# Performance work log

Measured on AMD Instinct MI355X. Metric: run time of the kernel, lower is better.

## Reference

```python
import jax, jax.numpy as jnp
import numpy as np

B, T = 1, 2048
N_EMBD = 2048
N_HEAD = 16
HEAD_DIM = 128
Q_COMP = 1536
KV_COMP = 512
ROT = 64  # rotate_dim


def setup_inputs() -> dict:
    key = jax.random.key(0)
    ks = jax.random.split(key, 12)
    nrm = lambda k, shp, sc=1.0: jax.random.normal(k, shp, jnp.float32) * sc
    return {
        "x": nrm(ks[0], (B, T, N_EMBD)),
        "cos": jax.random.uniform(ks[1], (T, ROT // 2), jnp.float32),
        "sin": jax.random.uniform(ks[2], (T, ROT // 2), jnp.float32),
        "Wq_d_w": nrm(ks[3], (Q_COMP, N_EMBD), 0.02),
        "Wq_d_b": jnp.zeros((Q_COMP,), jnp.float32),
        "Wkv_d_w": nrm(ks[4], (KV_COMP, N_EMBD), 0.02),
        "Wq_u_w": nrm(ks[5], (N_HEAD * HEAD_DIM, Q_COMP), 0.02),
        "Wk_u_w": nrm(ks[6], (N_HEAD * HEAD_DIM, KV_COMP), 0.02),
        "Wv_u_w": nrm(ks[7], (N_HEAD * HEAD_DIM, KV_COMP), 0.02),
        "W_qr_w": nrm(ks[8], (N_HEAD * ROT, Q_COMP), 0.02),
        "W_kr_w": nrm(ks[9], (ROT, N_EMBD), 0.02),
        "W_out_w": nrm(ks[10], (N_EMBD, N_HEAD * HEAD_DIM), 0.02),
    }


def _rope(x, cos, sin):
    # x: [B, H, T, r]; cos/sin: [T, r//2] broadcast over batch and heads
    d = x.shape[-1] // 2
    x1, x2 = x[..., :d], x[..., d:]
    return jnp.concatenate([x1 * cos + x2 * sin, -x1 * sin + x2 * cos], axis=-1)


def reference(x, cos, sin, Wq_d_w, Wq_d_b, Wkv_d_w, Wq_u_w, Wk_u_w, Wv_u_w, W_qr_w, W_kr_w, W_out_w):
    Bn, Tn, _ = x.shape
    cq = x @ Wq_d_w.T + Wq_d_b           # [B,T,Qc] latent query
    ckv = x @ Wkv_d_w.T                  # [B,T,Kc] compressed KV latent (= K_t = V)
    Wq_u = Wq_u_w.reshape(N_HEAD, HEAD_DIM, Q_COMP)
    Wk_u = Wk_u_w.reshape(N_HEAD, HEAD_DIM, KV_COMP)
    Wv_u = Wv_u_w.reshape(N_HEAD, HEAD_DIM, KV_COMP)
    # absorbed per-head W_qk[h] = Wq_u_h^T @ Wk_u_h : [H, Qc, Kc]
    W_qk = jnp.einsum('hdq,hdk->hqk', Wq_u, Wk_u)
    Q_t = jnp.einsum('btq,hqk->bhtk', cq, W_qk)   # [B,H,T,Kc] content query in latent space
    Q_r = _rope(jnp.einsum('btq,hrq->bhtr', cq, W_qr_w.reshape(N_HEAD, ROT, Q_COMP)), cos, sin)
    K_r = _rope((x @ W_kr_w.T)[:, None], cos, sin)  # [B,1,T,R] single shared rotary key head
    Q = jnp.concatenate([Q_t, Q_r], axis=-1)        # [B,H,T,Kc+R]
    K = jnp.concatenate([ckv[:, None], K_r], axis=-1)  # [B,1,T,Kc+R]
    scale = 1.0 / np.sqrt(KV_COMP + ROT).astype(np.float32)
    scores = jnp.einsum('bhqd,bokd->bhqk', Q, K) * scale  # [B,H,T,T]
    causal = jnp.tril(jnp.ones((Tn, Tn), dtype=bool))
    scores = jnp.where(causal, scores, jnp.asarray(-1e30, scores.dtype))
    probs = jax.nn.softmax(scores, axis=-1)
    attn = jnp.einsum('bhqk,bkc->bhqc', probs, ckv)  # [B,H,T,Kc] latent attention output
    # absorbed output projection: up-project per head via Wv_u, then W_out
    heads = jnp.einsum('bhtc,hdc->bthd', attn, Wv_u).reshape(Bn, Tn, N_HEAD * HEAD_DIM)
    return heads @ W_out_w.T                          # [B,T,C]
```

## Files before the change

kernel.cpp:

```cpp
#include <hip/hip_runtime.h>
#include <math.h>
#include <stdint.h>
#include <stddef.h>

typedef __bf16 bf16;
typedef __bf16 bf16x8 __attribute__((ext_vector_type(8)));
typedef __bf16 bf16x4 __attribute__((ext_vector_type(4)));
typedef __bf16 bf16x2 __attribute__((ext_vector_type(2)));
typedef float  f32x4  __attribute__((ext_vector_type(4)));
typedef float  f32x4v __attribute__((ext_vector_type(4)));

typedef __attribute__((address_space(1))) const void* as1cv;
typedef __attribute__((address_space(3))) void*       as3v;

__device__ __forceinline__ f32x4 mfma16(bf16x8 a, bf16x8 b, f32x4 c) {
  return __builtin_amdgcn_mfma_f32_16x16x32_bf16(a, b, c, 0, 0, 0);
}

__device__ __forceinline__ void gload_lds16(const bf16* g, bf16* l) {
  __builtin_amdgcn_global_load_lds((as1cv)g, (as3v)l, 16, 0, 0);
}

struct CvtTable {
  const float* s[9];
  bf16* d[9];
  int cum[10];
};

__global__ void cvt_all(CvtTable T, int total4) {
  int i = blockIdx.x * blockDim.x + threadIdx.x;
  int stride = gridDim.x * blockDim.x;
  for (; i < total4; i += stride) {
    int k = 0;
#pragma unroll
    for (int j = 1; j < 9; ++j) k += (i >= T.cum[j]) ? 1 : 0;
    int off = i - T.cum[k];
    f32x4v v = ((const f32x4v*)T.s[k])[off];
    bf16x4 o;
    o[0] = (bf16)v[0]; o[1] = (bf16)v[1]; o[2] = (bf16)v[2]; o[3] = (bf16)v[3];
    ((bf16x4*)T.d[k])[off] = o;
  }
}

__device__ __forceinline__ void gemm_core(
    const bf16* __restrict__ A, int lda,
    const bf16* __restrict__ B, int K,
    float* __restrict__ Cf, bf16* __restrict__ Cb, int ldc,
    const float* __restrict__ bias, int bias_n, int m0, int n0)
{
  __shared__ __align__(16) bf16 Al[2][128 * 64];
  __shared__ __align__(16) bf16 Bl[2][128 * 64];
  const int tid = threadIdx.x;
  const int l = tid & 63;
  const int wid = tid >> 6;
  const int wr = wid >> 2, wc = wid & 3;
  const int lr = l & 15, lg = l >> 4;

  const int ch0 = tid, ch1 = tid + 512;
  const int ar0 = ch0 >> 3, ap0 = (ch0 & 7) ^ (ar0 & 7);
  const int ar1 = ch1 >> 3, ap1 = (ch1 & 7) ^ (ar1 & 7);
  const bf16* pA0 = A + (size_t)(m0 + ar0) * lda + ap0 * 8;
  const bf16* pA1 = A + (size_t)(m0 + ar1) * lda + ap1 * 8;
  const bf16* pB0 = B + (size_t)(n0 + ar0) * K + ap0 * 8;
  const bf16* pB1 = B + (size_t)(n0 + ar1) * K + ap1 * 8;
  bf16* dA0[2] = { &Al[0][ch0 * 8], &Al[1][ch0 * 8] };
  bf16* dA1[2] = { &Al[0][ch1 * 8], &Al[1][ch1 * 8] };
  bf16* dB0[2] = { &Bl[0][ch0 * 8], &Bl[1][ch0 * 8] };
  bf16* dB1[2] = { &Bl[0][ch1 * 8], &Bl[1][ch1 * 8] };

  auto STAGE = [&](int b) {
    gload_lds16(pA0, b ? dA0[1] : dA0[0]);
    gload_lds16(pA1, b ? dA1[1] : dA1[0]);
    gload_lds16(pB0, b ? dB0[1] : dB0[0]);
    gload_lds16(pB1, b ? dB1[1] : dB1[0]);
    pA0 += 64; pA1 += 64; pB0 += 64; pB1 += 64;
  };

  f32x4 z = {0.f, 0.f, 0.f, 0.f};
  f32x4 acc[4][2];
#pragma unroll
  for (int i = 0; i < 4; ++i)
#pragma unroll
    for (int j = 0; j < 2; ++j) acc[i][j] = z;

  STAGE(0);
  int cur = 0;
  for (int k0 = 0; k0 < K; k0 += 64) {
    if (k0 + 64 < K) {
      STAGE(cur ^ 1);
      asm volatile("s_waitcnt vmcnt(4)" ::: "memory");
    } else {
      asm volatile("s_waitcnt vmcnt(0)" ::: "memory");
    }
    __builtin_amdgcn_s_barrier();
    __builtin_amdgcn_sched_barrier(0);
#pragma unroll
    for (int kk = 0; kk < 2; ++kk) {
      bf16x8 af[4], bfr[2];
#pragma unroll
      for (int i = 0; i < 4; ++i) {
        int row = wr * 64 + i * 16 + lr;
        int cq = kk * 4 + lg;
        af[i] = *(const bf16x8*)(&Al[cur][row * 64 + ((cq ^ (row & 7)) * 8)]);
      }
#pragma unroll
      for (int j = 0; j < 2; ++j) {
        int row = wc * 32 + j * 16 + lr;
        int cq = kk * 4 + lg;
        bfr[j] = *(const bf16x8*)(&Bl[cur][row * 64 + ((cq ^ (row & 7)) * 8)]);
      }
#pragma unroll
      for (int i = 0; i < 4; ++i)
#pragma unroll
        for (int j = 0; j < 2; ++j)
          acc[i][j] = mfma16(af[i], bfr[j], acc[i][j]);
    }
    __builtin_amdgcn_sched_barrier(0);
    __builtin_amdgcn_s_barrier();
    cur ^= 1;
  }

#pragma unroll
  for (int i = 0; i < 4; ++i)
#pragma unroll
    for (int j = 0; j < 2; ++j)
#pragma unroll
      for (int r = 0; r < 4; ++r) {
        int row = m0 + wr * 64 + i * 16 + lg * 4 + r;
        int col = n0 + wc * 32 + j * 16 + lr;
        float v = acc[i][j][r];
        if (bias != nullptr && col < bias_n) v += bias[col];
        if (Cf != nullptr) Cf[(size_t)row * ldc + col] = v;
        else               Cb[(size_t)row * ldc + col] = (bf16)v;
      }
}

template<bool OUTF32>
__global__ __launch_bounds__(512) void gemm_bt(
    const bf16* __restrict__ A, int lda,
    const bf16* __restrict__ B, int K,
    float* __restrict__ Cf, bf16* __restrict__ Cb, int ldc,
    const float* __restrict__ bias, int bias_n)
{
  gemm_core(A, lda, B, K, OUTF32 ? Cf : nullptr, Cb, ldc, bias, bias_n,
            blockIdx.y * 128, blockIdx.x * 128);
}

__global__ __launch_bounds__(512) void gemm_bt_dual(
    const bf16* __restrict__ A0, int lda0, const bf16* __restrict__ B0, int K0,
    bf16* __restrict__ C0, int ldc0, int nbx0,
    const bf16* __restrict__ A1, int lda1, const bf16* __restrict__ B1, int K1,
    bf16* __restrict__ C1, int ldc1, int nbx1)
{
  int bid = blockIdx.x;
  if (bid < nbx0 * 16) {
    gemm_core(A0, lda0, B0, K0, nullptr, C0, ldc0, nullptr, 0,
              (bid / nbx0) * 128, (bid % nbx0) * 128);
  } else {
    bid -= nbx0 * 16;
    gemm_core(A1, lda1, B1, K1, nullptr, C1, ldc1, nullptr, 0,
              (bid / nbx1) * 128, (bid % nbx1) * 128);
  }
}

__global__ void rope_tv(const bf16* __restrict__ QA, const bf16* __restrict__ c_all,
                        const float* __restrict__ cosb, const float* __restrict__ sinb,
                        bf16* __restrict__ Qr, bf16* __restrict__ Kr,
                        const bf16* __restrict__ KV, bf16* __restrict__ Vt)
{
  int bid = blockIdx.x;
  if (bid < 2048) {
    int t = bid;
    for (int idx = threadIdx.x; idx < 544; idx += 256) {
      if (idx < 512) {
        int h = idx >> 5, p = idx & 31;
        float x1 = (float)QA[(size_t)t * 3072 + 2048 + h * 64 + p];
        float x2 = (float)QA[(size_t)t * 3072 + 2048 + h * 64 + 32 + p];
        float c = cosb[t * 32 + p], s = sinb[t * 32 + p];
        Qr[(size_t)t * 1024 + h * 64 + p]      = (bf16)( x1 * c + x2 * s);
        Qr[(size_t)t * 1024 + h * 64 + 32 + p] = (bf16)(-x1 * s + x2 * c);
      } else {
        int p = idx - 512;
        float x1 = (float)c_all[(size_t)t * 2176 + 2048 + p];
        float x2 = (float)c_all[(size_t)t * 2176 + 2048 + 32 + p];
        float c = cosb[t * 32 + p], s = sinb[t * 32 + p];
        Kr[(size_t)t * 64 + p]      = (bf16)( x1 * c + x2 * s);
        Kr[(size_t)t * 64 + 32 + p] = (bf16)(-x1 * s + x2 * c);
      }
    }
  } else {
    __shared__ bf16 tile[32][33];
    int tb = bid - 2048;
    int t0 = (tb & 63) * 32, c0 = (tb >> 6) * 32;
    int tx = threadIdx.x & 31, ty = threadIdx.x >> 5;
#pragma unroll
    for (int r = 0; r < 4; ++r)
      tile[ty + r * 8][tx] = KV[(size_t)(t0 + ty + r * 8) * 4096 + 2048 + c0 + tx];
    __syncthreads();
#pragma unroll
    for (int r = 0; r < 4; ++r)
      Vt[(size_t)(c0 + ty + r * 8) * 2048 + t0 + tx] = tile[tx][ty + r * 8];
  }
}

__global__ __launch_bounds__(256) void attn_kernel(
    const bf16* __restrict__ QA,
    const bf16* __restrict__ Qr,
    const bf16* __restrict__ KV,
    const bf16* __restrict__ Kr,
    const bf16* __restrict__ Vt,
    bf16* __restrict__ heads)
{
  __shared__ __align__(16) bf16 Kl[2][32 * 128];
  __shared__ __align__(16) bf16 Krl[2][32 * 64];
  __shared__ __align__(16) bf16 Vl[2][128 * 32];
  __shared__ __align__(16) bf16 Pl[4][16][40];

  const int tid = threadIdx.x;
  const int l = tid & 63;
  const int wid = tid >> 6;
  const int lr = l & 15, lg = l >> 4;

  const int wg = blockIdx.x;
  const int xcd = wg & 7, inx = wg >> 3;
  const int half = inx >> 5, j = inx & 31;
  const int h = xcd * 2 + half;
  const int qb = half ? j : 31 - j;
  const int q0 = qb * 64 + wid * 16;
  const int q = q0 + lr;

  const float scale = 0.041666666666666664f;
  f32x4 z = {0.f, 0.f, 0.f, 0.f};

  const int chK0 = tid, chK1 = tid + 256;
  const int rK0 = chK0 >> 4, pK0 = chK0 & 15;
  const int rK1 = chK1 >> 4, pK1 = chK1 & 15;
  const int cbK0 = (pK0 & 8) | ((pK0 & 7) ^ (rK0 & 7));
  const int cbK1 = (pK1 & 8) | ((pK1 & 7) ^ (rK1 & 7));
  const bf16* gK0 = &KV[(size_t)rK0 * 4096 + h * 128 + cbK0 * 8];
  const bf16* gK1 = &KV[(size_t)rK1 * 4096 + h * 128 + cbK1 * 8];
  const int rKr = tid >> 3, pKr = tid & 7, cbKr = pKr ^ (rKr & 7);
  const bf16* gKr = &Kr[(size_t)rKr * 64 + cbKr * 8];
  const int chV0 = tid, chV1 = tid + 256;
  const int rV0 = chV0 >> 2, pV0 = chV0 & 3, cbV0 = pV0 ^ ((rV0 >> 1) & 3);
  const int rV1 = chV1 >> 2, pV1 = chV1 & 3, cbV1 = pV1 ^ ((rV1 >> 1) & 3);
  const bf16* gV0 = &Vt[(size_t)(h * 128 + rV0) * 2048 + cbV0 * 8];
  const bf16* gV1 = &Vt[(size_t)(h * 128 + rV1) * 2048 + cbV1 * 8];
  bf16* dK0[2] = { &Kl[0][chK0 * 8], &Kl[1][chK0 * 8] };
  bf16* dK1[2] = { &Kl[0][chK1 * 8], &Kl[1][chK1 * 8] };
  bf16* dKr[2] = { &Krl[0][tid * 8], &Krl[1][tid * 8] };
  bf16* dV0[2] = { &Vl[0][chV0 * 8], &Vl[1][chV0 * 8] };
  bf16* dV1[2] = { &Vl[0][chV1 * 8], &Vl[1][chV1 * 8] };

  auto STAGE = [&](int b) {
    gload_lds16(gK0, b ? dK0[1] : dK0[0]);
    gload_lds16(gK1, b ? dK1[1] : dK1[0]);
    gload_lds16(gKr, b ? dKr[1] : dKr[0]);
    gload_lds16(gV0, b ? dV0[1] : dV0[0]);
    gload_lds16(gV1, b ? dV1[1] : dV1[0]);
    gK0 += 32 * 4096; gK1 += 32 * 4096; gKr += 32 * 64; gV0 += 32; gV1 += 32;
  };

  bf16x8 aq[6];
#pragma unroll
  for (int kc = 0; kc < 4; ++kc)
    aq[kc] = *(const bf16x8*)&QA[(size_t)q * 3072 + h * 128 + kc * 32 + lg * 8];
#pragma unroll
  for (int kc = 4; kc < 6; ++kc)
    aq[kc] = *(const bf16x8*)&Qr[(size_t)q * 1024 + h * 64 + (kc - 4) * 32 + lg * 8];

  float m_run = -1e30f, l_run = 0.f;
  f32x4 acc[8];
#pragma unroll
  for (int c = 0; c < 8; ++c) acc[c] = z;

  const int nIter = 2 * qb + 2;
  STAGE(0);
  int cur = 0;
  for (int st = 0; st < nIter; ++st) {
    const int s0 = st * 32;
    if (st + 1 < nIter) {
      STAGE(cur ^ 1);
      asm volatile("s_waitcnt vmcnt(5)" ::: "memory");
    } else {
      asm volatile("s_waitcnt vmcnt(0)" ::: "memory");
    }
    __builtin_amdgcn_s_barrier();
    __builtin_amdgcn_sched_barrier(0);
    if (s0 <= q0 + 15) {
      f32x4 sc[2];
      sc[0] = z; sc[1] = z;
#pragma unroll
      for (int t = 0; t < 2; ++t) {
        const int rr = t * 16 + lr;
#pragma unroll
        for (int kc = 0; kc < 4; ++kc) {
          int g = kc * 4 + lg;
          bf16x8 ka = *(const bf16x8*)&Kl[cur][rr * 128 + (((g & 8) | ((g & 7) ^ (rr & 7))) * 8)];
          sc[t] = mfma16(ka, aq[kc], sc[t]);
        }
#pragma unroll
        for (int kc = 4; kc < 6; ++kc) {
          int g = (kc - 4) * 4 + lg;
          bf16x8 ka = *(const bf16x8*)&Krl[cur][rr * 64 + ((g ^ (rr & 7)) * 8)];
          sc[t] = mfma16(ka, aq[kc], sc[t]);
        }
      }
      float pv[2][4];
      float mx = -1e30f;
      if (s0 + 31 > q0) {
#pragma unroll
        for (int t = 0; t < 2; ++t)
#pragma unroll
          for (int r = 0; r < 4; ++r) {
            int k = s0 + t * 16 + lg * 4 + r;
            float v = sc[t][r] * scale;
            if (k > q) v = -1e30f;
            pv[t][r] = v;
            mx = fmaxf(mx, v);
          }
      } else {
#pragma unroll
        for (int t = 0; t < 2; ++t)
#pragma unroll
          for (int r = 0; r < 4; ++r) {
            float v = sc[t][r] * scale;
            pv[t][r] = v;
            mx = fmaxf(mx, v);
          }
      }
      mx = fmaxf(mx, __shfl_xor(mx, 16, 64));
      mx = fmaxf(mx, __shfl_xor(mx, 32, 64));
      if (!__all(mx - m_run <= 8.f)) {
        float mnew = fmaxf(m_run, mx);
        float alpha = __expf(m_run - mnew);
        l_run *= alpha;
#pragma unroll
        for (int c = 0; c < 8; ++c)
#pragma unroll
          for (int r = 0; r < 4; ++r) acc[c][r] *= alpha;
        m_run = mnew;
      }
      float sum = 0.f;
#pragma unroll
      for (int t = 0; t < 2; ++t)
#pragma unroll
        for (int r = 0; r < 4; ++r) {
          float e = __expf(pv[t][r] - m_run);
          pv[t][r] = e;
          sum += e;
        }
      sum += __shfl_xor(sum, 16, 64);
      sum += __shfl_xor(sum, 32, 64);
      l_run += sum;
#pragma unroll
      for (int t = 0; t < 2; ++t)
#pragma unroll
        for (int hf = 0; hf < 2; ++hf) {
          bf16x2 w;
          w[0] = (bf16)pv[t][2 * hf];
          w[1] = (bf16)pv[t][2 * hf + 1];
          *(bf16x2*)&Pl[wid][lr][t * 16 + lg * 4 + 2 * hf] = w;
        }
      bf16x8 pa = *(const bf16x8*)&Pl[wid][lr][lg * 8];
#pragma unroll
      for (int c = 0; c < 8; ++c) {
        int rv = c * 16 + lr;
        bf16x8 va = *(const bf16x8*)&Vl[cur][rv * 32 + ((lg ^ ((rv >> 1) & 3)) * 8)];
        acc[c] = mfma16(va, pa, acc[c]);
      }
    }
    __builtin_amdgcn_sched_barrier(0);
    __builtin_amdgcn_s_barrier();
    cur ^= 1;
  }

  const float inv = 1.f / l_run;
#pragma unroll
  for (int c = 0; c < 8; ++c) {
    bf16x4 o;
#pragma unroll
    for (int r = 0; r < 4; ++r) o[r] = (bf16)(acc[c][r] * inv);
    *(bf16x4*)&heads[(size_t)q * 2048 + h * 128 + c * 16 + lg * 4] = o;
  }
}

extern "C" void kernel_launch(void* const* d_in, const int* in_sizes, int n_in,
                              void* d_out, int out_size, void* d_ws, size_t ws_size,
                              hipStream_t stream) {
  (void)in_sizes; (void)n_in; (void)out_size; (void)ws_size;
  const float* x      = (const float*)d_in[0];
  const float* cosp   = (const float*)d_in[1];
  const float* sinp   = (const float*)d_in[2];
  const float* Wq_d   = (const float*)d_in[3];
  const float* Wq_d_b = (const float*)d_in[4];
  const float* Wkv_d  = (const float*)d_in[5];
  const float* Wq_u   = (const float*)d_in[6];
  const float* Wk_u   = (const float*)d_in[7];
  const float* Wv_u   = (const float*)d_in[8];
  const float* W_qr   = (const float*)d_in[9];
  const float* W_kr   = (const float*)d_in[10];
  const float* W_out  = (const float*)d_in[11];

  char* ws = (char*)d_ws;
  size_t off = 0;
  auto alloc = [&](size_t bytes) {
    char* p = ws + off;
    off += (bytes + 255) & ~(size_t)255;
    return p;
  };
  bf16* xb    = (bf16*)alloc((size_t)2048 * 2048 * 2);
  bf16* Wcat  = (bf16*)alloc((size_t)2176 * 2048 * 2);
  bf16* c_all = (bf16*)alloc((size_t)2048 * 2176 * 2);
  bf16* Wqu   = (bf16*)alloc((size_t)3072 * 1536 * 2);
  bf16* QA    = (bf16*)alloc((size_t)2048 * 3072 * 2);
  bf16* Wkvu  = (bf16*)alloc((size_t)4096 * 512 * 2);
  bf16* KV    = (bf16*)alloc((size_t)2048 * 4096 * 2);
  bf16* Qr    = (bf16*)alloc((size_t)2048 * 1024 * 2);
  bf16* Kr    = (bf16*)alloc((size_t)2048 * 64 * 2);
  bf16* Wout  = (bf16*)alloc((size_t)2048 * 2048 * 2);
  bf16* Vt    = xb;
  bf16* heads = Wqu;

  CvtTable T;
  const float* srcs[9] = { x, Wq_d, Wkv_d, W_kr, Wq_u, W_qr, Wk_u, Wv_u, W_out };
  bf16* dsts[9] = { xb, Wcat, Wcat + (size_t)1536 * 2048, Wcat + (size_t)2048 * 2048,
                    Wqu, Wqu + (size_t)2048 * 1536, Wkvu, Wkvu + (size_t)2048 * 512, Wout };
  size_t ns[9] = { (size_t)2048 * 2048, (size_t)1536 * 2048, (size_t)512 * 2048,
                   (size_t)64 * 2048, (size_t)2048 * 1536, (size_t)1024 * 1536,
                   (size_t)2048 * 512, (size_t)2048 * 512, (size_t)2048 * 2048 };
  int cum = 0;
  for (int i = 0; i < 9; ++i) {
    T.s[i] = srcs[i]; T.d[i] = dsts[i]; T.cum[i] = cum;
    cum += (int)(ns[i] / 4);
  }
  T.cum[9] = cum;
  cvt_all<<<2048, 256, 0, stream>>>(T, cum);

  gemm_bt<false><<<dim3(17, 16), 512, 0, stream>>>(xb, 2048, Wcat, 2048,
                                                   nullptr, c_all, 2176, Wq_d_b, 1536);
  gemm_bt_dual<<<24 * 16 + 32 * 16, 512, 0, stream>>>(
      c_all, 2176, Wqu, 1536, QA, 3072, 24,
      c_all + 1536, 2176, Wkvu, 512, KV, 4096, 32);
  rope_tv<<<2048 + 4096, 256, 0, stream>>>(QA, c_all, cosp, sinp, Qr, Kr, KV, Vt);
  attn_kernel<<<512, 256, 0, stream>>>(QA, Qr, KV, Kr, Vt, heads);
  gemm_bt<true><<<dim3(16, 16), 512, 0, stream>>>(heads, 2048, Wout, 2048,
                                                  (float*)d_out, nullptr, 2048, nullptr, 0);
}
```

Measured before the change: 318.5 us.

## Split-K the down and output GEMMs and retile attention into 32-row blocks

The two large GEMMs are split along K into two grid halves that write partial results, followed by separate reduction kernels (adding the bias for the query latent). The GEMM inner loop replaces the manual vmcnt waits with plain __syncthreads, which may reduce load/compute overlap. The attention kernel now uses 128-thread blocks covering 32 query rows with a balanced causal ordering, a unified LDS buffer for K, rotary K and V, and register shuffles in place of the LDS round-trip for P. The partial-sum scheme doubles grid occupancy but adds extra kernels and partial-sum memory traffic, and the first GEMM's partials are rounded to bf16 before summation.

```diff
diff --git a/kernel.cpp b/kernel.cpp
--- a/kernel.cpp
+++ b/kernel.cpp
@@ -44,7 +44,7 @@
 
 __device__ __forceinline__ void gemm_core(
     const bf16* __restrict__ A, int lda,
-    const bf16* __restrict__ B, int K,
+    const bf16* __restrict__ B, int ldb, int Klen,
     float* __restrict__ Cf, bf16* __restrict__ Cb, int ldc,
     const float* __restrict__ bias, int bias_n, int m0, int n0)
 {
@@ -61,8 +61,8 @@
   const int ar1 = ch1 >> 3, ap1 = (ch1 & 7) ^ (ar1 & 7);
   const bf16* pA0 = A + (size_t)(m0 + ar0) * lda + ap0 * 8;
   const bf16* pA1 = A + (size_t)(m0 + ar1) * lda + ap1 * 8;
-  const bf16* pB0 = B + (size_t)(n0 + ar0) * K + ap0 * 8;
-  const bf16* pB1 = B + (size_t)(n0 + ar1) * K + ap1 * 8;
+  const bf16* pB0 = B + (size_t)(n0 + ar0) * ldb + ap0 * 8;
+  const bf16* pB1 = B + (size_t)(n0 + ar1) * ldb + ap1 * 8;
   bf16* dA0[2] = { &Al[0][ch0 * 8], &Al[1][ch0 * 8] };
   bf16* dA1[2] = { &Al[0][ch1 * 8], &Al[1][ch1 * 8] };
   bf16* dB0[2] = { &Bl[0][ch0 * 8], &Bl[1][ch0 * 8] };
@@ -84,16 +84,10 @@
     for (int j = 0; j < 2; ++j) acc[i][j] = z;
 
   STAGE(0);
+  __syncthreads();
   int cur = 0;
-  for (int k0 = 0; k0 < K; k0 += 64) {
-    if (k0 + 64 < K) {
-      STAGE(cur ^ 1);
-      asm volatile("s_waitcnt vmcnt(4)" ::: "memory");
-    } else {
-      asm volatile("s_waitcnt vmcnt(0)" ::: "memory");
-    }
-    __builtin_amdgcn_s_barrier();
-    __builtin_amdgcn_sched_barrier(0);
+  for (int k0 = 0; k0 < Klen; k0 += 64) {
+    if (k0 + 64 < Klen) STAGE(cur ^ 1);
 #pragma unroll
     for (int kk = 0; kk < 2; ++kk) {
       bf16x8 af[4], bfr[2];
@@ -115,8 +109,7 @@
         for (int j = 0; j < 2; ++j)
           acc[i][j] = mfma16(af[i], bfr[j], acc[i][j]);
     }
-    __builtin_amdgcn_sched_barrier(0);
-    __builtin_amdgcn_s_barrier();
+    __syncthreads();
     cur ^= 1;
   }
 
@@ -136,14 +129,17 @@
 }
 
 template<bool OUTF32>
-__global__ __launch_bounds__(512) void gemm_bt(
+__global__ __launch_bounds__(512) void gemm_splitk(
     const bf16* __restrict__ A, int lda,
-    const bf16* __restrict__ B, int K,
-    float* __restrict__ Cf, bf16* __restrict__ Cb, int ldc,
-    const float* __restrict__ bias, int bias_n)
-{
-  gemm_core(A, lda, B, K, OUTF32 ? Cf : nullptr, Cb, ldc, bias, bias_n,
-            blockIdx.y * 128, blockIdx.x * 128);
+    const bf16* __restrict__ B, int ldb, int Khalf,
+    float* __restrict__ F0, float* __restrict__ F1,
+    bf16* __restrict__ H0, bf16* __restrict__ H1, int ldc)
+{
+  int zz = blockIdx.z;
+  gemm_core(A + zz * Khalf, lda, B + zz * Khalf, ldb, Khalf,
+            OUTF32 ? (zz ? F1 : F0) : nullptr,
+            OUTF32 ? nullptr : (zz ? H1 : H0), ldc,
+            nullptr, 0, blockIdx.y * 128, blockIdx.x * 128);
 }
 
 __global__ __launch_bounds__(512) void gemm_bt_dual(
@@ -154,12 +150,50 @@
 {
   int bid = blockIdx.x;
   if (bid < nbx0 * 16) {
-    gemm_core(A0, lda0, B0, K0, nullptr, C0, ldc0, nullptr, 0,
+    gemm_core(A0, lda0, B0, K0, K0, nullptr, C0, ldc0, nullptr, 0,
               (bid / nbx0) * 128, (bid % nbx0) * 128);
   } else {
     bid -= nbx0 * 16;
-    gemm_core(A1, lda1, B1, K1, nullptr, C1, ldc1, nullptr, 0,
+    gemm_core(A1, lda1, B1, K1, K1, nullptr, C1, ldc1, nullptr, 0,
               (bid / nbx1) * 128, (bid % nbx1) * 128);
+  }
+}
+
+__global__ void reduce_c(const bf16* __restrict__ P0, const bf16* __restrict__ P1,
+                         const float* __restrict__ bias, bf16* __restrict__ c_all)
+{
+  const int n8 = 2048 * 2176 / 8;
+  int i = blockIdx.x * blockDim.x + threadIdx.x;
+  int stride = gridDim.x * blockDim.x;
+  for (; i < n8; i += stride) {
+    int col8 = (i % 272) * 8;
+    bf16x8 a = ((const bf16x8*)P0)[i];
+    bf16x8 b = ((const bf16x8*)P1)[i];
+    bf16x8 o;
+    if (col8 < 1536) {
+#pragma unroll
+      for (int j = 0; j < 8; ++j)
+        o[j] = (bf16)((float)a[j] + (float)b[j] + bias[col8 + j]);
+    } else {
+#pragma unroll
+      for (int j = 0; j < 8; ++j)
+        o[j] = (bf16)((float)a[j] + (float)b[j]);
+    }
+    ((bf16x8*)c_all)[i] = o;
+  }
+}
+
+__global__ void reduce_f(const float* __restrict__ P0, const float* __restrict__ P1,
+                         float* __restrict__ out)
+{
+  const int n4 = 2048 * 2048 / 4;
+  int i = blockIdx.x * blockDim.x + threadIdx.x;
+  int stride = gridDim.x * blockDim.x;
+  for (; i < n4; i += stride) {
+    f32x4v a = ((const f32x4v*)P0)[i];
+    f32x4v b = ((const f32x4v*)P1)[i];
+    f32x4v o = a + b;
+    ((f32x4v*)out)[i] = o;
   }
 }
 
@@ -203,7 +237,7 @@
   }
 }
 
-__global__ __launch_bounds__(256) void attn_kernel(
+__global__ __launch_bounds__(128) void attn_kernel(
     const bf16* __restrict__ QA,
     const bf16* __restrict__ Qr,
     const bf16* __restrict__ KV,
@@ -211,10 +245,7 @@
     const bf16* __restrict__ Vt,
     bf16* __restrict__ heads)
 {
-  __shared__ __align__(16) bf16 Kl[2][32 * 128];
-  __shared__ __align__(16) bf16 Krl[2][32 * 64];
-  __shared__ __align__(16) bf16 Vl[2][128 * 32];
-  __shared__ __align__(16) bf16 Pl[4][16][40];
+  __shared__ __align__(16) bf16 L[2][10240];
 
   const int tid = threadIdx.x;
   const int l = tid & 63;
@@ -223,42 +254,46 @@
 
   const int wg = blockIdx.x;
   const int xcd = wg & 7, inx = wg >> 3;
-  const int half = inx >> 5, j = inx & 31;
-  const int h = xcd * 2 + half;
-  const int qb = half ? j : 31 - j;
-  const int q0 = qb * 64 + wid * 16;
+  const int rnd = inx >> 5, c = inx & 31;
+  const int h = xcd * 2 + (rnd >> 1);
+  const int qt = (rnd == 0) ? (63 - c) : (rnd == 1) ? (31 - c) : (rnd == 2) ? c : (32 + c);
+  const int q0 = qt * 32 + wid * 16;
   const int q = q0 + lr;
 
   const float scale = 0.041666666666666664f;
   f32x4 z = {0.f, 0.f, 0.f, 0.f};
 
-  const int chK0 = tid, chK1 = tid + 256;
-  const int rK0 = chK0 >> 4, pK0 = chK0 & 15;
-  const int rK1 = chK1 >> 4, pK1 = chK1 & 15;
-  const int cbK0 = (pK0 & 8) | ((pK0 & 7) ^ (rK0 & 7));
-  const int cbK1 = (pK1 & 8) | ((pK1 & 7) ^ (rK1 & 7));
-  const bf16* gK0 = &KV[(size_t)rK0 * 4096 + h * 128 + cbK0 * 8];
-  const bf16* gK1 = &KV[(size_t)rK1 * 4096 + h * 128 + cbK1 * 8];
-  const int rKr = tid >> 3, pKr = tid & 7, cbKr = pKr ^ (rKr & 7);
-  const bf16* gKr = &Kr[(size_t)rKr * 64 + cbKr * 8];
-  const int chV0 = tid, chV1 = tid + 256;
-  const int rV0 = chV0 >> 2, pV0 = chV0 & 3, cbV0 = pV0 ^ ((rV0 >> 1) & 3);
-  const int rV1 = chV1 >> 2, pV1 = chV1 & 3, cbV1 = pV1 ^ ((rV1 >> 1) & 3);
-  const bf16* gV0 = &Vt[(size_t)(h * 128 + rV0) * 2048 + cbV0 * 8];
-  const bf16* gV1 = &Vt[(size_t)(h * 128 + rV1) * 2048 + cbV1 * 8];
-  bf16* dK0[2] = { &Kl[0][chK0 * 8], &Kl[1][chK0 * 8] };
-  bf16* dK1[2] = { &Kl[0][chK1 * 8], &Kl[1][chK1 * 8] };
-  bf16* dKr[2] = { &Krl[0][tid * 8], &Krl[1][tid * 8] };
-  bf16* dV0[2] = { &Vl[0][chV0 * 8], &Vl[1][chV0 * 8] };
-  bf16* dV1[2] = { &Vl[0][chV1 * 8], &Vl[1][chV1 * 8] };
+  const bf16* gK[6]; int sK[6]; int chK[6];
+#pragma unroll
+  for (int i = 0; i < 6; ++i) {
+    int ch = i * 128 + tid;
+    int row = ch / 24, gcol = ch - row * 24;
+    int lgc = (gcol & 24) | ((gcol & 7) ^ (row & 7));
+    if (lgc < 16) { gK[i] = KV + (size_t)row * 4096 + h * 128 + lgc * 8; sK[i] = 32 * 4096; }
+    else          { gK[i] = Kr + (size_t)row * 64 + (lgc - 16) * 8;      sK[i] = 32 * 64; }
+    chK[i] = ch;
+  }
+  const bf16* gV[4]; int chV[4];
+#pragma unroll
+  for (int j = 0; j < 4; ++j) {
+    int ch = j * 128 + tid;
+    int r = ch >> 2, p = ch & 3;
+    int cb = p ^ ((r >> 1) & 3);
+    gV[j] = Vt + (size_t)(h * 128 + r) * 2048 + cb * 8;
+    chV[j] = ch;
+  }
 
   auto STAGE = [&](int b) {
-    gload_lds16(gK0, b ? dK0[1] : dK0[0]);
-    gload_lds16(gK1, b ? dK1[1] : dK1[0]);
-    gload_lds16(gKr, b ? dKr[1] : dKr[0]);
-    gload_lds16(gV0, b ? dV0[1] : dV0[0]);
-    gload_lds16(gV1, b ? dV1[1] : dV1[0]);
-    gK0 += 32 * 4096; gK1 += 32 * 4096; gKr += 32 * 64; gV0 += 32; gV1 += 32;
+#pragma unroll
+    for (int i = 0; i < 6; ++i) {
+      gload_lds16(gK[i], &L[b][chK[i] * 8]);
+      gK[i] += sK[i];
+    }
+#pragma unroll
+    for (int j = 0; j < 4; ++j) {
+      gload_lds16(gV[j], &L[b][6144 + chV[j] * 8]);
+      gV[j] += 32;
+    }
   };
 
   bf16x8 aq[6];
@@ -269,107 +304,126 @@
   for (int kc = 4; kc < 6; ++kc)
     aq[kc] = *(const bf16x8*)&Qr[(size_t)q * 1024 + h * 64 + (kc - 4) * 32 + lg * 8];
 
+  const int sl0 = lr + 16 * ((lg & 1) * 2);
+  const int sl1 = sl0 + 16;
+  const bool hiT = (lg >> 1) != 0;
+
   float m_run = -1e30f, l_run = 0.f;
   f32x4 acc[8];
 #pragma unroll
-  for (int c = 0; c < 8; ++c) acc[c] = z;
-
-  const int nIter = 2 * qb + 2;
+  for (int cc = 0; cc < 8; ++cc) acc[cc] = z;
+
+  const int nIter = qt + 1;
   STAGE(0);
   int cur = 0;
   for (int st = 0; st < nIter; ++st) {
     const int s0 = st * 32;
     if (st + 1 < nIter) {
       STAGE(cur ^ 1);
-      asm volatile("s_waitcnt vmcnt(5)" ::: "memory");
+      asm volatile("s_waitcnt vmcnt(10)" ::: "memory");
     } else {
       asm volatile("s_waitcnt vmcnt(0)" ::: "memory");
     }
     __builtin_amdgcn_s_barrier();
     __builtin_amdgcn_sched_barrier(0);
-    if (s0 <= q0 + 15) {
-      f32x4 sc[2];
-      sc[0] = z; sc[1] = z;
-#pragma unroll
-      for (int t = 0; t < 2; ++t) {
-        const int rr = t * 16 + lr;
-#pragma unroll
-        for (int kc = 0; kc < 4; ++kc) {
-          int g = kc * 4 + lg;
-          bf16x8 ka = *(const bf16x8*)&Kl[cur][rr * 128 + (((g & 8) | ((g & 7) ^ (rr & 7))) * 8)];
-          sc[t] = mfma16(ka, aq[kc], sc[t]);
+
+    f32x4 scA[2], scB[2];
+    scA[0] = z; scA[1] = z; scB[0] = z; scB[1] = z;
+#pragma unroll
+    for (int t = 0; t < 2; ++t) {
+      const int rr = t * 16 + lr;
+#pragma unroll
+      for (int kc = 0; kc < 6; ++kc) {
+        int g = kc * 4 + lg;
+        int gc = (g & 24) | ((g & 7) ^ (rr & 7));
+        bf16x8 ka = *(const bf16x8*)&L[cur][rr * 192 + gc * 8];
+        if (kc < 3) scA[t] = mfma16(ka, aq[kc], scA[t]);
+        else        scB[t] = mfma16(ka, aq[kc], scB[t]);
+      }
+    }
+    bf16x8 va[8];
+#pragma unroll
+    for (int cc = 0; cc < 8; ++cc) {
+      int rv = cc * 16 + lr;
+      va[cc] = *(const bf16x8*)&L[cur][6144 + rv * 32 + ((lg ^ ((rv >> 1) & 3)) * 8)];
+    }
+    f32x4 sc[2];
+    sc[0] = scA[0] + scB[0];
+    sc[1] = scA[1] + scB[1];
+
+    float pv[2][4];
+    float mx = -1e30f;
+    if (s0 + 31 > q0) {
+#pragma unroll
+      for (int t = 0; t < 2; ++t)
+#pragma unroll
+        for (int r = 0; r < 4; ++r) {
+          int k = s0 + t * 16 + lg * 4 + r;
+          float v = sc[t][r] * scale;
+          if (k > q) v = -1e30f;
+          pv[t][r] = v;
+          mx = fmaxf(mx, v);
         }
-#pragma unroll
-        for (int kc = 4; kc < 6; ++kc) {
-          int g = (kc - 4) * 4 + lg;
-          bf16x8 ka = *(const bf16x8*)&Krl[cur][rr * 64 + ((g ^ (rr & 7)) * 8)];
-          sc[t] = mfma16(ka, aq[kc], sc[t]);
+    } else {
+#pragma unroll
+      for (int t = 0; t < 2; ++t)
+#pragma unroll
+        for (int r = 0; r < 4; ++r) {
+          float v = sc[t][r] * scale;
+          pv[t][r] = v;
+          mx = fmaxf(mx, v);
         }
-      }
-      float pv[2][4];
-      float mx = -1e30f;
-      if (s0 + 31 > q0) {
-#pragma unroll
-        for (int t = 0; t < 2; ++t)
-#pragma unroll
-          for (int r = 0; r < 4; ++r) {
-            int k = s0 + t * 16 + lg * 4 + r;
-            float v = sc[t][r] * scale;
-            if (k > q) v = -1e30f;
-            pv[t][r] = v;
-            mx = fmaxf(mx, v);
-          }
-      } else {
-#pragma unroll
-        for (int t = 0; t < 2; ++t)
-#pragma unroll
-          for (int r = 0; r < 4; ++r) {
-            float v = sc[t][r] * scale;
-            pv[t][r] = v;
-            mx = fmaxf(mx, v);
-          }
-      }
-      mx = fmaxf(mx, __shfl_xor(mx, 16, 64));
-      mx = fmaxf(mx, __shfl_xor(mx, 32, 64));
-      if (!__all(mx - m_run <= 8.f)) {
-        float mnew = fmaxf(m_run, mx);
-        float alpha = __expf(m_run - mnew);
-        l_run *= alpha;
-#pragma unroll
-        for (int c = 0; c < 8; ++c)
-#pragma unroll
-          for (int r = 0; r < 4; ++r) acc[c][r] *= alpha;
-        m_run = mnew;
-      }
-      float sum = 0.f;
-#pragma unroll
-      for (int t = 0; t < 2; ++t)
-#pragma unroll
-        for (int r = 0; r < 4; ++r) {
-          float e = __expf(pv[t][r] - m_run);
-          pv[t][r] = e;
-          sum += e;
-        }
-      sum += __shfl_xor(sum, 16, 64);
-      sum += __shfl_xor(sum, 32, 64);
-      l_run += sum;
-#pragma unroll
-      for (int t = 0; t < 2; ++t)
-#pragma unroll
-        for (int hf = 0; hf < 2; ++hf) {
-          bf16x2 w;
-          w[0] = (bf16)pv[t][2 * hf];
-          w[1] = (bf16)pv[t][2 * hf + 1];
-          *(bf16x2*)&Pl[wid][lr][t * 16 + lg * 4 + 2 * hf] = w;
-        }
-      bf16x8 pa = *(const bf16x8*)&Pl[wid][lr][lg * 8];
-#pragma unroll
-      for (int c = 0; c < 8; ++c) {
-        int rv = c * 16 + lr;
-        bf16x8 va = *(const bf16x8*)&Vl[cur][rv * 32 + ((lg ^ ((rv >> 1) & 3)) * 8)];
-        acc[c] = mfma16(va, pa, acc[c]);
-      }
-    }
+    }
+    mx = fmaxf(mx, __shfl_xor(mx, 16, 64));
+    mx = fmaxf(mx, __shfl_xor(mx, 32, 64));
+    if (!__all(mx - m_run <= 8.f)) {
+      float mnew = fmaxf(m_run, mx);
+      float alpha = __expf(m_run - mnew);
+      l_run *= alpha;
+#pragma unroll
+      for (int cc = 0; cc < 8; ++cc)
+#pragma unroll
+        for (int r = 0; r < 4; ++r) acc[cc][r] *= alpha;
+      m_run = mnew;
+    }
+    float sum = 0.f;
+#pragma unroll
+    for (int t = 0; t < 2; ++t)
+#pragma unroll
+      for (int r = 0; r < 4; ++r) {
+        float e = __expf(pv[t][r] - m_run);
+        pv[t][r] = e;
+        sum += e;
+      }
+    sum += __shfl_xor(sum, 16, 64);
+    sum += __shfl_xor(sum, 32, 64);
+    l_run += sum;
+
+    union { bf16x2 h2; int u; } wv[2][2];
+#pragma unroll
+    for (int t = 0; t < 2; ++t)
+#pragma unroll
+      for (int hf = 0; hf < 2; ++hf) {
+        wv[t][hf].h2[0] = (bf16)pv[t][2 * hf];
+        wv[t][hf].h2[1] = (bf16)pv[t][2 * hf + 1];
+      }
+    union { int u[4]; bf16x8 v; } pa;
+    {
+      int a0, a1;
+      a0 = __shfl(wv[0][0].u, sl0, 64); a1 = __shfl(wv[1][0].u, sl0, 64);
+      pa.u[0] = hiT ? a1 : a0;
+      a0 = __shfl(wv[0][1].u, sl0, 64); a1 = __shfl(wv[1][1].u, sl0, 64);
+      pa.u[1] = hiT ? a1 : a0;
+      a0 = __shfl(wv[0][0].u, sl1, 64); a1 = __shfl(wv[1][0].u, sl1, 64);
+      pa.u[2] = hiT ? a1 : a0;
+      a0 = __shfl(wv[0][1].u, sl1, 64); a1 = __shfl(wv[1][1].u, sl1, 64);
+      pa.u[3] = hiT ? a1 : a0;
+    }
+
+#pragma unroll
+    for (int cc = 0; cc < 8; ++cc)
+      acc[cc] = mfma16(va[cc], pa.v, acc[cc]);
+
     __builtin_amdgcn_sched_barrier(0);
     __builtin_amdgcn_s_barrier();
     cur ^= 1;
@@ -377,11 +431,11 @@
 
   const float inv = 1.f / l_run;
 #pragma unroll
-  for (int c = 0; c < 8; ++c) {
+  for (int cc = 0; cc < 8; ++cc) {
     bf16x4 o;
 #pragma unroll
-    for (int r = 0; r < 4; ++r) o[r] = (bf16)(acc[c][r] * inv);
-    *(bf16x4*)&heads[(size_t)q * 2048 + h * 128 + c * 16 + lg * 4] = o;
+    for (int r = 0; r < 4; ++r) o[r] = (bf16)(acc[cc][r] * inv);
+    *(bf16x4*)&heads[(size_t)q * 2048 + h * 128 + cc * 16 + lg * 4] = o;
   }
 }
 
@@ -421,6 +475,10 @@
   bf16* Wout  = (bf16*)alloc((size_t)2048 * 2048 * 2);
   bf16* Vt    = xb;
   bf16* heads = Wqu;
+  bf16* P0b   = QA;
+  bf16* P1b   = KV;
+  float* P0f  = (float*)xb;
+  float* P1f  = (float*)QA;
 
   CvtTable T;
   const float* srcs[9] = { x, Wq_d, Wkv_d, W_kr, Wq_u, W_qr, Wk_u, Wv_u, W_out };
@@ -437,13 +495,15 @@
   T.cum[9] = cum;
   cvt_all<<<2048, 256, 0, stream>>>(T, cum);
 
-  gemm_bt<false><<<dim3(17, 16), 512, 0, stream>>>(xb, 2048, Wcat, 2048,
-                                                   nullptr, c_all, 2176, Wq_d_b, 1536);
+  gemm_splitk<false><<<dim3(17, 16, 2), 512, 0, stream>>>(
+      xb, 2048, Wcat, 2048, 1024, nullptr, nullptr, P0b, P1b, 2176);
+  reduce_c<<<2176, 256, 0, stream>>>(P0b, P1b, Wq_d_b, c_all);
   gemm_bt_dual<<<24 * 16 + 32 * 16, 512, 0, stream>>>(
       c_all, 2176, Wqu, 1536, QA, 3072, 24,
       c_all + 1536, 2176, Wkvu, 512, KV, 4096, 32);
   rope_tv<<<2048 + 4096, 256, 0, stream>>>(QA, c_all, cosp, sinp, Qr, Kr, KV, Vt);
-  attn_kernel<<<512, 256, 0, stream>>>(QA, Qr, KV, Kr, Vt, heads);
-  gemm_bt<true><<<dim3(16, 16), 512, 0, stream>>>(heads, 2048, Wout, 2048,
-                                                  (float*)d_out, nullptr, 2048, nullptr, 0);
-}
+  attn_kernel<<<1024, 128, 0, stream>>>(QA, Qr, KV, Kr, Vt, heads);
+  gemm_splitk<true><<<dim3(16, 16, 2), 512, 0, stream>>>(
+      heads, 2048, Wout, 2048, 1024, P0f, P1f, nullptr, nullptr, 2048);
+  reduce_f<<<2048, 256, 0, stream>>>(P0f, P1f, (float*)d_out);
+}
```

Result: no change. 323.7 us (+1.6%).
